# Kernel optimization log

Measured on AMD Instinct MI355X. Metric: run time of the kernel, lower is better.

Reference implementation:

```python
import jax, jax.numpy as jnp
import numpy as np

B, S, HID = 2, 2048, 1024
H, KVH, D = 16, 4, 64
N_REP = H // KVH
SCALE = D ** -0.5
CAP = 50.0


def rotate_half(x):
    x1, x2 = x[..., : D // 2], x[..., D // 2 :]
    return jnp.concatenate((-x2, x1), axis=-1)


def setup_inputs() -> dict:
    key = jax.random.key(0)
    ks = jax.random.split(key, 10)
    X = jax.random.normal(ks[0], (B, S, HID), dtype=jnp.float32)
    # RoPE tables: (B, S, D)
    inv_freq = 1.0 / (10000.0 ** (np.arange(0, D, 2, dtype=np.float32) / D))
    pos = np.arange(S, dtype=np.float32)
    freqs = np.outer(pos, inv_freq)  # (S, D/2)
    emb = np.concatenate([freqs, freqs], axis=-1)  # (S, D)
    cos = jnp.broadcast_to(jnp.asarray(np.cos(emb)), (B, S, D))
    sin = jnp.broadcast_to(jnp.asarray(np.sin(emb)), (B, S, D))
    # causal mask: 1 where key <= query
    mask = jnp.broadcast_to(jnp.tril(jnp.ones((S, S), dtype=jnp.int32)), (B, S, S))
    std = HID ** -0.5
    Wq = jax.random.normal(ks[1], (HID, HID), dtype=jnp.float32) * std
    bq = jnp.zeros((HID,), dtype=jnp.float32)
    Wk = jax.random.normal(ks[2], (KVH * D, HID), dtype=jnp.float32) * std
    bk = jnp.zeros((KVH * D,), dtype=jnp.float32)
    Wv = jax.random.normal(ks[3], (KVH * D, HID), dtype=jnp.float32) * std
    bv = jnp.zeros((KVH * D,), dtype=jnp.float32)
    Wo = jax.random.normal(ks[4], (HID, HID), dtype=jnp.float32) * std
    bo = jnp.zeros((HID,), dtype=jnp.float32)
    return {"X": X, "cos": cos, "sin": sin, "mask": mask,
            "Wq": Wq, "bq": bq, "Wk": Wk, "bk": bk,
            "Wv": Wv, "bv": bv, "Wo": Wo, "bo": bo}


def reference(X, cos, sin, mask, Wq, bq, Wk, bk, Wv, bv, Wo, bo):
    bsz, q_len, _ = X.shape
    q = (X @ Wq.T + bq).reshape(bsz, q_len, H, D).transpose(0, 2, 1, 3)    # (B,H,S,D)
    k = (X @ Wk.T + bk).reshape(bsz, q_len, KVH, D).transpose(0, 2, 1, 3)  # (B,KVH,S,D)
    v = (X @ Wv.T + bv).reshape(bsz, q_len, KVH, D).transpose(0, 2, 1, 3)
    c = cos[:, None, :, :]  # (B,1,S,D)
    s = sin[:, None, :, :]
    q = q * c + rotate_half(q) * s
    k = k * c + rotate_half(k) * s
    k = jnp.repeat(k, N_REP, axis=1)  # GQA expand -> (B,H,S,D)
    v = jnp.repeat(v, N_REP, axis=1)
    scores = jnp.einsum('bhqd,bhkd->bhqk', q, k) * SCALE
    scores = jnp.clip(scores, -CAP, CAP)  # attention cap
    scores = jnp.where(mask[:, None, :, :] == 0, -1e9, scores)
    attn = jax.nn.softmax(scores, axis=-1)  # dropout p=0 -> identity
    ctx = jnp.einsum('bhqk,bhkd->bhqd', attn, v)
    ctx = ctx.transpose(0, 2, 1, 3).reshape(bsz, q_len, H * D)
    out = ctx @ Wo.T + bo
    return (out, attn)
```

## Files before the change

kernel.cpp:

```cpp
#include <hip/hip_runtime.h>
#include <cstdint>
#include <cstddef>

#define S_LEN   2048
#define BATCH   2
#define HID_DIM 1024
#define NHEAD   16
#define NKV     4
#define DHEAD   64
#define SCALE_F 0.125f
#define L2E     1.44269504f
#define QSCALE  (SCALE_F * L2E)
#define CAPL2   (50.0f * L2E)

typedef unsigned short u16;
typedef __attribute__((ext_vector_type(8))) short  short8_t;
typedef __attribute__((ext_vector_type(4))) float  f32x4;
typedef __attribute__((ext_vector_type(4))) u16    u16x4;

static __device__ __forceinline__ u16 f2bf(float f) {
  uint32_t x = __builtin_bit_cast(uint32_t, f);
  x += 0x7fffu + ((x >> 16) & 1u);
  return (u16)(x >> 16);
}

static __device__ __forceinline__ void gload_lds16(const void* g, void* l) {
  __builtin_amdgcn_global_load_lds((const __attribute__((address_space(1))) void*)g,
                                   (__attribute__((address_space(3))) void*)l, 16, 0, 0);
}

static __device__ __forceinline__ float expclamp2(float x) {
  return __builtin_amdgcn_exp2f(__builtin_amdgcn_fmed3f(x, -CAPL2, CAPL2) - CAPL2);
}

__global__ void cast_all(const float* __restrict__ X,  u16* __restrict__ xb,
                         const float* __restrict__ Wq, u16* __restrict__ wqb,
                         const float* __restrict__ Wk, u16* __restrict__ wkb,
                         const float* __restrict__ Wv, u16* __restrict__ wvb,
                         const float* __restrict__ Wo, u16* __restrict__ wob) {
  const float* src; u16* dst; int n4;
  switch (blockIdx.y) {
    case 0:  src = X;  dst = xb;  n4 = (BATCH * S_LEN * HID_DIM) / 4; break;
    case 1:  src = Wq; dst = wqb; n4 = (HID_DIM * HID_DIM) / 4;       break;
    case 2:  src = Wk; dst = wkb; n4 = (NKV * DHEAD * HID_DIM) / 4;   break;
    case 3:  src = Wv; dst = wvb; n4 = (NKV * DHEAD * HID_DIM) / 4;   break;
    default: src = Wo; dst = wob; n4 = (HID_DIM * HID_DIM) / 4;       break;
  }
  for (int i = blockIdx.x * 256 + threadIdx.x; i < n4; i += gridDim.x * 256) {
    f32x4 v = ((const f32x4*)src)[i];
    u16x4 o;
    o[0] = f2bf(v[0]); o[1] = f2bf(v[1]); o[2] = f2bf(v[2]); o[3] = f2bf(v[3]);
    ((u16x4*)dst)[i] = o;
  }
}

__global__ __launch_bounds__(256) void gemm_qkv(const u16* __restrict__ Xb,
                                                const u16* __restrict__ Wqb,
                                                const u16* __restrict__ Wkb,
                                                const u16* __restrict__ Wvb,
                                                const float* __restrict__ bq,
                                                const float* __restrict__ bk,
                                                const float* __restrict__ bv,
                                                const float* __restrict__ cosb,
                                                const float* __restrict__ sinb,
                                                u16* __restrict__ qout,
                                                u16* __restrict__ kout,
                                                u16* __restrict__ vtout) {
  __shared__ u16 As[128 * 64];
  __shared__ u16 Bs[128 * 64];
  const int tid = threadIdx.x, lane = tid & 63, wid = tid >> 6;
  const int l15 = lane & 15, lg = lane >> 4;
  const int m0 = blockIdx.x * 128, n0 = blockIdx.y * 128;
  const int wm = wid & 1, wn = wid >> 1;
  const int K = HID_DIM;

  const u16* Wp; const float* biasp; int nl, mode;
  if (n0 < 1024)      { Wp = Wqb; biasp = bq; nl = n0;        mode = 0; }
  else if (n0 < 1280) { Wp = Wkb; biasp = bk; nl = n0 - 1024; mode = 1; }
  else                { Wp = Wvb; biasp = bv; nl = n0 - 1280; mode = 2; }

  f32x4 acc[4][4];
  #pragma unroll
  for (int a = 0; a < 4; ++a)
    #pragma unroll
    for (int b2 = 0; b2 < 4; ++b2) acc[a][b2] = (f32x4){0.f, 0.f, 0.f, 0.f};

  const int srow = (lane >> 3), sg = (lane & 7);

  for (int kk = 0; kk < K; kk += 64) {
    __syncthreads();
    #pragma unroll
    for (int i = 0; i < 4; ++i) {
      const int c = wid * 4 + i;
      const int r = c * 8 + srow;
      const int g = sg ^ (r & 7);
      gload_lds16(Xb + (size_t)(m0 + r) * K + kk + g * 8, As + c * 512);
      gload_lds16(Wp + (size_t)(nl + r) * K + kk + g * 8, Bs + c * 512);
    }
    __syncthreads();
    #pragma unroll
    for (int ks = 0; ks < 2; ++ks) {
      short8_t xa[4], wb[4];
      #pragma unroll
      for (int f = 0; f < 4; ++f) {
        const int rm = wm * 64 + f * 16 + l15;
        const int rn = wn * 64 + f * 16 + l15;
        xa[f] = *(const short8_t*)(As + rm * 64 + (((ks * 4 + lg) ^ (rm & 7)) * 8));
        wb[f] = *(const short8_t*)(Bs + rn * 64 + (((ks * 4 + lg) ^ (rn & 7)) * 8));
      }
      if (mode != 2) {
        #pragma unroll
        for (int fn = 0; fn < 4; ++fn)
          #pragma unroll
          for (int fm = 0; fm < 4; ++fm)
            acc[fn][fm] = __builtin_amdgcn_mfma_f32_16x16x32_bf16(wb[fn], xa[fm], acc[fn][fm], 0, 0, 0);
      } else {
        #pragma unroll
        for (int fn = 0; fn < 4; ++fn)
          #pragma unroll
          for (int fm = 0; fm < 4; ++fm)
            acc[fn][fm] = __builtin_amdgcn_mfma_f32_16x16x32_bf16(xa[fm], wb[fn], acc[fn][fm], 0, 0, 0);
      }
    }
  }

  const int m_base = m0 + wm * 64;
  const int nlb = nl + wn * 64;

  if (mode < 2) {
    const int Nout = (mode == 0) ? HID_DIM : (NKV * DHEAD);
    const float qs = (mode == 0) ? QSCALE : 1.0f;
    u16* outb = (mode == 0) ? qout : kout;
    #pragma unroll
    for (int fm = 0; fm < 4; ++fm) {
      const int row = m_base + fm * 16 + l15;
      #pragma unroll
      for (int fn = 0; fn < 2; ++fn) {
        const int dh = fn * 16 + lg * 4;
        const f32x4 c4 = *(const f32x4*)(cosb + (size_t)row * 64 + dh);
        const f32x4 s4 = *(const f32x4*)(sinb + (size_t)row * 64 + dh);
        f32x4 x1 = acc[fn][fm]     + *(const f32x4*)(biasp + nlb + fn * 16 + lg * 4);
        f32x4 x2 = acc[fn + 2][fm] + *(const f32x4*)(biasp + nlb + (fn + 2) * 16 + lg * 4);
        f32x4 o1 = (x1 * c4 - x2 * s4) * qs;
        f32x4 o2 = (x2 * c4 + x1 * s4) * qs;
        u16x4 u1, u2;
        #pragma unroll
        for (int i = 0; i < 4; ++i) { u1[i] = f2bf(o1[i]); u2[i] = f2bf(o2[i]); }
        *(u16x4*)(outb + (size_t)row * Nout + nlb + fn * 16 + lg * 4)       = u1;
        *(u16x4*)(outb + (size_t)row * Nout + nlb + (fn + 2) * 16 + lg * 4) = u2;
      }
    }
  } else {
    #pragma unroll
    for (int fn = 0; fn < 4; ++fn) {
      const int d = nlb + fn * 16 + l15;
      const float bvs = biasp[d];
      #pragma unroll
      for (int fm = 0; fm < 4; ++fm) {
        const int s0 = m_base + fm * 16 + lg * 4;
        const int b_ = s0 >> 11, s_ = s0 & (S_LEN - 1);
        u16x4 o;
        #pragma unroll
        for (int i = 0; i < 4; ++i) o[i] = f2bf(acc[fn][fm][i] + bvs);
        *(u16x4*)(vtout + (size_t)(b_ * 256 + d) * S_LEN + s_) = o;
      }
    }
  }
}

__global__ __launch_bounds__(256) void gemm_out(const u16* __restrict__ A,
                                                const u16* __restrict__ W,
                                                const float* __restrict__ bias,
                                                float* __restrict__ outp) {
  __shared__ u16 As[128 * 64];
  __shared__ u16 Bs[128 * 64];
  const int tid = threadIdx.x, lane = tid & 63, wid = tid >> 6;
  const int l15 = lane & 15, lg = lane >> 4;
  const int m0 = blockIdx.x * 128, n0 = blockIdx.y * 128;
  const int wm = wid & 1, wn = wid >> 1;
  const int K = HID_DIM, N = HID_DIM;

  f32x4 acc[4][4];
  #pragma unroll
  for (int a = 0; a < 4; ++a)
    #pragma unroll
    for (int b2 = 0; b2 < 4; ++b2) acc[a][b2] = (f32x4){0.f, 0.f, 0.f, 0.f};

  const int srow = (lane >> 3), sg = (lane & 7);

  for (int kk = 0; kk < K; kk += 64) {
    __syncthreads();
    #pragma unroll
    for (int i = 0; i < 4; ++i) {
      const int c = wid * 4 + i;
      const int r = c * 8 + srow;
      const int g = sg ^ (r & 7);
      gload_lds16(A + (size_t)(m0 + r) * K + kk + g * 8, As + c * 512);
      gload_lds16(W + (size_t)(n0 + r) * K + kk + g * 8, Bs + c * 512);
    }
    __syncthreads();
    #pragma unroll
    for (int ks = 0; ks < 2; ++ks) {
      short8_t xa[4], wb[4];
      #pragma unroll
      for (int f = 0; f < 4; ++f) {
        const int rm = wm * 64 + f * 16 + l15;
        const int rn = wn * 64 + f * 16 + l15;
        xa[f] = *(const short8_t*)(As + rm * 64 + (((ks * 4 + lg) ^ (rm & 7)) * 8));
        wb[f] = *(const short8_t*)(Bs + rn * 64 + (((ks * 4 + lg) ^ (rn & 7)) * 8));
      }
      #pragma unroll
      for (int fn = 0; fn < 4; ++fn)
        #pragma unroll
        for (int fm = 0; fm < 4; ++fm)
          acc[fn][fm] = __builtin_amdgcn_mfma_f32_16x16x32_bf16(wb[fn], xa[fm], acc[fn][fm], 0, 0, 0);
    }
  }

  const int m_base = m0 + wm * 64, n_base = n0 + wn * 64;
  #pragma unroll
  for (int fn = 0; fn < 4; ++fn) {
    const int col = n_base + fn * 16 + lg * 4;
    const f32x4 bvv = *(const f32x4*)(bias + col);
    #pragma unroll
    for (int fm = 0; fm < 4; ++fm) {
      const int row = m_base + fm * 16 + l15;
      *(f32x4*)(outp + (size_t)row * N + col) = acc[fn][fm] + bvv;
    }
  }
}

__global__ __launch_bounds__(256) void attn_fused(const u16* __restrict__ qb,
                                                  const u16* __restrict__ kb,
                                                  const u16* __restrict__ vtb,
                                                  float* __restrict__ attn,
                                                  u16* __restrict__ ctxb) {
  __shared__ u16 kS[2][64 * 64];
  __shared__ u16 vS[2][64 * 64];
  __shared__ u16 pS[4][16][72];

  const int tid = threadIdx.x, lane = tid & 63, wid = tid >> 6;
  const int l15 = lane & 15, lg = lane >> 4;
  const int bh = blockIdx.x, b = bh >> 4, h = bh & 15, kvh = h >> 2;
  const int qt = (int)(gridDim.y - 1 - blockIdx.y);
  const int q0 = qt * 64;
  const int NT = qt + 1;
  const int qw = q0 + wid * 16;
  const int qrow = qw + l15;

  const u16* qp = qb + (size_t)(b * S_LEN + qrow) * HID_DIM + h * DHEAD + lg * 8;
  const short8_t qf0 = *(const short8_t*)qp;
  const short8_t qf1 = *(const short8_t*)(qp + 32);

  const u16* kbase  = kb  + (size_t)(b * S_LEN) * (NKV * DHEAD) + kvh * DHEAD;
  const u16* vtbase = vtb + (size_t)(b * NKV + kvh) * DHEAD * S_LEN;

  const int sr8 = wid * 8 + (lane >> 3);
  const int sgr = lane & 7;

  auto stageK = [&](int bi, int kv0) {
    #pragma unroll
    for (int it = 0; it < 2; ++it) {
      const int r = it * 32 + sr8;
      const int g = sgr ^ (r & 7);
      gload_lds16(kbase + (size_t)(kv0 + r) * (NKV * DHEAD) + g * 8,
                  &kS[bi][(it * 32 + wid * 8) * 64]);
    }
  };
  auto stageV = [&](int bi, int kv0) {
    #pragma unroll
    for (int it = 0; it < 2; ++it) {
      const int r = it * 32 + sr8;
      const int g = sgr ^ (r & 7);
      gload_lds16(vtbase + (size_t)r * S_LEN + kv0 + g * 8,
                  &vS[bi][(it * 32 + wid * 8) * 64]);
    }
  };

  f32x4 lacc = (f32x4){0.f, 0.f, 0.f, 0.f};
  stageK(0, 0);
  for (int t = 0; t < NT; ++t) {
    const int kv0 = t * 64;
    if (t + 1 < NT) {
      stageK((t + 1) & 1, kv0 + 64);
      asm volatile("s_waitcnt vmcnt(2)" ::: "memory");
    } else {
      asm volatile("s_waitcnt vmcnt(0)" ::: "memory");
    }
    __builtin_amdgcn_s_barrier();
    const u16* ks = kS[t & 1];
    const bool maskc = (kv0 + 63 > qw);
    #pragma unroll
    for (int g16 = 0; g16 < 4; ++g16) {
      const int r = g16 * 16 + l15;
      short8_t ka0 = *(const short8_t*)(ks + r * 64 + ((lg ^ (r & 7)) * 8));
      short8_t ka1 = *(const short8_t*)(ks + r * 64 + (((4 + lg) ^ (r & 7)) * 8));
      f32x4 sacc = (f32x4){0.f, 0.f, 0.f, 0.f};
      sacc = __builtin_amdgcn_mfma_f32_16x16x32_bf16(ka0, qf0, sacc, 0, 0, 0);
      sacc = __builtin_amdgcn_mfma_f32_16x16x32_bf16(ka1, qf1, sacc, 0, 0, 0);
      #pragma unroll
      for (int i = 0; i < 4; ++i) {
        float e = expclamp2(sacc[i]);
        if (maskc) {
          const int kvi = kv0 + g16 * 16 + lg * 4 + i;
          e = (kvi <= qrow) ? e : 0.f;
        }
        lacc[i] += e;
      }
    }
    __builtin_amdgcn_s_barrier();
  }
  float lsum = (lacc[0] + lacc[1]) + (lacc[2] + lacc[3]);
  lsum += __shfl_xor(lsum, 16);
  lsum += __shfl_xor(lsum, 32);
  const float invl = 1.f / lsum;

  float* abase = attn + (size_t)bh * S_LEN * S_LEN;
  float* arow  = abase + (size_t)qrow * S_LEN;
  f32x4 ctx[4];
  #pragma unroll
  for (int dt = 0; dt < 4; ++dt) ctx[dt] = (f32x4){0.f, 0.f, 0.f, 0.f};

  stageK(0, 0);
  stageV(0, 0);
  for (int t = 0; t < NT; ++t) {
    const int kv0 = t * 64;
    if (t + 1 < NT) {
      stageK((t + 1) & 1, kv0 + 64);
      stageV((t + 1) & 1, kv0 + 64);
      asm volatile("s_waitcnt vmcnt(4)" ::: "memory");
    } else {
      asm volatile("s_waitcnt vmcnt(0)" ::: "memory");
    }
    __builtin_amdgcn_s_barrier();
    const u16* ks = kS[t & 1];
    const u16* vs = vS[t & 1];
    const bool maskc = (kv0 + 63 > qw);
    #pragma unroll
    for (int g16 = 0; g16 < 4; ++g16) {
      const int r = g16 * 16 + l15;
      short8_t ka0 = *(const short8_t*)(ks + r * 64 + ((lg ^ (r & 7)) * 8));
      short8_t ka1 = *(const short8_t*)(ks + r * 64 + (((4 + lg) ^ (r & 7)) * 8));
      f32x4 sacc = (f32x4){0.f, 0.f, 0.f, 0.f};
      sacc = __builtin_amdgcn_mfma_f32_16x16x32_bf16(ka0, qf0, sacc, 0, 0, 0);
      sacc = __builtin_amdgcn_mfma_f32_16x16x32_bf16(ka1, qf1, sacc, 0, 0, 0);
      f32x4 pv; u16x4 pb;
      #pragma unroll
      for (int i = 0; i < 4; ++i) {
        float e = expclamp2(sacc[i]);
        if (maskc) {
          const int kvi = kv0 + g16 * 16 + lg * 4 + i;
          e = (kvi <= qrow) ? e : 0.f;
        }
        float p = e * invl;
        pv[i] = p;
        pb[i] = f2bf(p);
      }
      *(f32x4*)(arow + kv0 + g16 * 16 + lg * 4) = pv;
      *(u16x4*)&pS[wid][l15][g16 * 16 + lg * 4] = pb;
    }
    short8_t pa0 = *(const short8_t*)&pS[wid][l15][lg * 8];
    short8_t pa1 = *(const short8_t*)&pS[wid][l15][32 + lg * 8];
    #pragma unroll
    for (int dt = 0; dt < 4; ++dt) {
      const int r = dt * 16 + l15;
      short8_t bv0 = *(const short8_t*)(vs + r * 64 + ((lg ^ (r & 7)) * 8));
      short8_t bv1 = *(const short8_t*)(vs + r * 64 + (((4 + lg) ^ (r & 7)) * 8));
      ctx[dt] = __builtin_amdgcn_mfma_f32_16x16x32_bf16(bv0, pa0, ctx[dt], 0, 0, 0);
      ctx[dt] = __builtin_amdgcn_mfma_f32_16x16x32_bf16(bv1, pa1, ctx[dt], 0, 0, 0);
    }
    __builtin_amdgcn_s_barrier();
  }

  #pragma unroll
  for (int dt = 0; dt < 4; ++dt) {
    u16x4 o;
    #pragma unroll
    for (int i = 0; i < 4; ++i) o[i] = f2bf(ctx[dt][i]);
    *(u16x4*)(ctxb + (size_t)(b * S_LEN + qrow) * HID_DIM + h * DHEAD + dt * 16 + lg * 4) = o;
  }

  const int zc0 = q0 + 64;
  if (zc0 < S_LEN) {
    const f32x4 z = (f32x4){0.f, 0.f, 0.f, 0.f};
    for (int r = wid; r < 64; r += 4) {
      float* rowp = abase + (size_t)(q0 + r) * S_LEN;
      for (int c = zc0 + lane * 4; c < S_LEN; c += 256)
        *(f32x4*)(rowp + c) = z;
    }
  }
}

extern "C" void kernel_launch(void* const* d_in, const int* in_sizes, int n_in,
                              void* d_out, int out_size, void* d_ws, size_t ws_size,
                              hipStream_t stream) {
  (void)in_sizes; (void)n_in; (void)out_size; (void)ws_size;
  const float* X    = (const float*)d_in[0];
  const float* cosb = (const float*)d_in[1];
  const float* sinb = (const float*)d_in[2];
  const float* Wq = (const float*)d_in[4];
  const float* bq = (const float*)d_in[5];
  const float* Wk = (const float*)d_in[6];
  const float* bk = (const float*)d_in[7];
  const float* Wv = (const float*)d_in[8];
  const float* bv = (const float*)d_in[9];
  const float* Wo = (const float*)d_in[10];
  const float* bo = (const float*)d_in[11];

  float* outp  = (float*)d_out;
  float* attnp = outp + (size_t)BATCH * S_LEN * HID_DIM;

  const int M = BATCH * S_LEN;
  u16* ws    = (u16*)d_ws;
  u16* Xb    = ws;
  u16* Wqb   = Xb  + (size_t)M * HID_DIM;
  u16* Wkb   = Wqb + (size_t)HID_DIM * HID_DIM;
  u16* Wvb   = Wkb + (size_t)NKV * DHEAD * HID_DIM;
  u16* Wob   = Wvb + (size_t)NKV * DHEAD * HID_DIM;
  u16* qbuf  = Wob + (size_t)HID_DIM * HID_DIM;
  u16* kbuf  = qbuf + (size_t)M * HID_DIM;
  u16* vtbuf = kbuf + (size_t)M * NKV * DHEAD;
  u16* ctxb  = vtbuf + (size_t)M * NKV * DHEAD;

  cast_all<<<dim3(1024, 5), 256, 0, stream>>>(X, Xb, Wq, Wqb, Wk, Wkb, Wv, Wvb, Wo, Wob);

  gemm_qkv<<<dim3(M / 128, 12), 256, 0, stream>>>(Xb, Wqb, Wkb, Wvb, bq, bk, bv,
                                                  cosb, sinb, qbuf, kbuf, vtbuf);

  attn_fused<<<dim3(BATCH * NHEAD, S_LEN / 64), 256, 0, stream>>>(qbuf, kbuf, vtbuf, attnp, ctxb);

  gemm_out<<<dim3(M / 128, HID_DIM / 128), 256, 0, stream>>>(ctxb, Wob, bo, outp);
}
```

Before: 235.9 us.

## Process two 64-row query sub-tiles per attention block to reuse K/V tiles

Each attention workgroup now handles 128 query rows, split into two 64-row sub-tiles A and B, so every staged K/V tile in shared memory feeds twice as many MFMAs. This halves the grid and the redundant global-to-LDS K/V traffic. Sub-tile A skips compute on fully masked KV tiles and writes zeros to the attention matrix there instead. The trade-offs are more registers per thread, fewer blocks (reduced occupancy and parallelism), and worse load balance across the causal triangle.

```diff
diff --git a/kernel.cpp b/kernel.cpp
--- a/kernel.cpp
+++ b/kernel.cpp
@@ -237,20 +237,23 @@
                                                   u16* __restrict__ ctxb) {
   __shared__ u16 kS[2][64 * 64];
   __shared__ u16 vS[2][64 * 64];
-  __shared__ u16 pS[4][16][72];
+  __shared__ u16 pS[4][2][16][72];
 
   const int tid = threadIdx.x, lane = tid & 63, wid = tid >> 6;
   const int l15 = lane & 15, lg = lane >> 4;
   const int bh = blockIdx.x, b = bh >> 4, h = bh & 15, kvh = h >> 2;
   const int qt = (int)(gridDim.y - 1 - blockIdx.y);
-  const int q0 = qt * 64;
-  const int NT = qt + 1;
-  const int qw = q0 + wid * 16;
-  const int qrow = qw + l15;
-
-  const u16* qp = qb + (size_t)(b * S_LEN + qrow) * HID_DIM + h * DHEAD + lg * 8;
-  const short8_t qf0 = *(const short8_t*)qp;
-  const short8_t qf1 = *(const short8_t*)(qp + 32);
+  const int q0 = qt * 128;
+  const int NT = 2 * qt + 2;
+  const int qwA = q0 + wid * 16;
+  const int qwB = qwA + 64;
+
+  const u16* qpA = qb + (size_t)(b * S_LEN + qwA + l15) * HID_DIM + h * DHEAD + lg * 8;
+  const u16* qpB = qb + (size_t)(b * S_LEN + qwB + l15) * HID_DIM + h * DHEAD + lg * 8;
+  const short8_t qfA0 = *(const short8_t*)qpA;
+  const short8_t qfA1 = *(const short8_t*)(qpA + 32);
+  const short8_t qfB0 = *(const short8_t*)qpB;
+  const short8_t qfB1 = *(const short8_t*)(qpB + 32);
 
   const u16* kbase  = kb  + (size_t)(b * S_LEN) * (NKV * DHEAD) + kvh * DHEAD;
   const u16* vtbase = vtb + (size_t)(b * NKV + kvh) * DHEAD * S_LEN;
@@ -277,7 +280,8 @@
     }
   };
 
-  f32x4 lacc = (f32x4){0.f, 0.f, 0.f, 0.f};
+  f32x4 laccA = (f32x4){0.f, 0.f, 0.f, 0.f};
+  f32x4 laccB = (f32x4){0.f, 0.f, 0.f, 0.f};
   stageK(0, 0);
   for (int t = 0; t < NT; ++t) {
     const int kv0 = t * 64;
@@ -289,37 +293,58 @@
     }
     __builtin_amdgcn_s_barrier();
     const u16* ks = kS[t & 1];
-    const bool maskc = (kv0 + 63 > qw);
+    const bool actA = (kv0 <= qwA + 15);
+    const bool mA = (kv0 + 63 > qwA), mB = (kv0 + 63 > qwB);
     #pragma unroll
     for (int g16 = 0; g16 < 4; ++g16) {
       const int r = g16 * 16 + l15;
       short8_t ka0 = *(const short8_t*)(ks + r * 64 + ((lg ^ (r & 7)) * 8));
       short8_t ka1 = *(const short8_t*)(ks + r * 64 + (((4 + lg) ^ (r & 7)) * 8));
-      f32x4 sacc = (f32x4){0.f, 0.f, 0.f, 0.f};
-      sacc = __builtin_amdgcn_mfma_f32_16x16x32_bf16(ka0, qf0, sacc, 0, 0, 0);
-      sacc = __builtin_amdgcn_mfma_f32_16x16x32_bf16(ka1, qf1, sacc, 0, 0, 0);
+      f32x4 sB = (f32x4){0.f, 0.f, 0.f, 0.f};
+      sB = __builtin_amdgcn_mfma_f32_16x16x32_bf16(ka0, qfB0, sB, 0, 0, 0);
+      sB = __builtin_amdgcn_mfma_f32_16x16x32_bf16(ka1, qfB1, sB, 0, 0, 0);
       #pragma unroll
       for (int i = 0; i < 4; ++i) {
-        float e = expclamp2(sacc[i]);
-        if (maskc) {
+        float e = expclamp2(sB[i]);
+        if (mB) {
           const int kvi = kv0 + g16 * 16 + lg * 4 + i;
-          e = (kvi <= qrow) ? e : 0.f;
+          e = (kvi <= qwB + l15) ? e : 0.f;
         }
-        lacc[i] += e;
+        laccB[i] += e;
+      }
+      if (actA) {
+        f32x4 sA = (f32x4){0.f, 0.f, 0.f, 0.f};
+        sA = __builtin_amdgcn_mfma_f32_16x16x32_bf16(ka0, qfA0, sA, 0, 0, 0);
+        sA = __builtin_amdgcn_mfma_f32_16x16x32_bf16(ka1, qfA1, sA, 0, 0, 0);
+        #pragma unroll
+        for (int i = 0; i < 4; ++i) {
+          float e = expclamp2(sA[i]);
+          if (mA) {
+            const int kvi = kv0 + g16 * 16 + lg * 4 + i;
+            e = (kvi <= qwA + l15) ? e : 0.f;
+          }
+          laccA[i] += e;
+        }
       }
     }
     __builtin_amdgcn_s_barrier();
   }
-  float lsum = (lacc[0] + lacc[1]) + (lacc[2] + lacc[3]);
-  lsum += __shfl_xor(lsum, 16);
-  lsum += __shfl_xor(lsum, 32);
-  const float invl = 1.f / lsum;
+  float lsA = (laccA[0] + laccA[1]) + (laccA[2] + laccA[3]);
+  float lsB = (laccB[0] + laccB[1]) + (laccB[2] + laccB[3]);
+  lsA += __shfl_xor(lsA, 16); lsA += __shfl_xor(lsA, 32);
+  lsB += __shfl_xor(lsB, 16); lsB += __shfl_xor(lsB, 32);
+  const float invlA = 1.f / lsA;
+  const float invlB = 1.f / lsB;
 
   float* abase = attn + (size_t)bh * S_LEN * S_LEN;
-  float* arow  = abase + (size_t)qrow * S_LEN;
-  f32x4 ctx[4];
+  float* arowA = abase + (size_t)(qwA + l15) * S_LEN;
+  float* arowB = abase + (size_t)(qwB + l15) * S_LEN;
+  f32x4 ctxA[4], ctxB[4];
   #pragma unroll
-  for (int dt = 0; dt < 4; ++dt) ctx[dt] = (f32x4){0.f, 0.f, 0.f, 0.f};
+  for (int dt = 0; dt < 4; ++dt) {
+    ctxA[dt] = (f32x4){0.f, 0.f, 0.f, 0.f};
+    ctxB[dt] = (f32x4){0.f, 0.f, 0.f, 0.f};
+  }
 
   stageK(0, 0);
   stageV(0, 0);
@@ -335,55 +360,88 @@
     __builtin_amdgcn_s_barrier();
     const u16* ks = kS[t & 1];
     const u16* vs = vS[t & 1];
-    const bool maskc = (kv0 + 63 > qw);
+    const bool actA = (kv0 <= qwA + 15);
+    const bool mA = (kv0 + 63 > qwA), mB = (kv0 + 63 > qwB);
+
     #pragma unroll
     for (int g16 = 0; g16 < 4; ++g16) {
       const int r = g16 * 16 + l15;
       short8_t ka0 = *(const short8_t*)(ks + r * 64 + ((lg ^ (r & 7)) * 8));
       short8_t ka1 = *(const short8_t*)(ks + r * 64 + (((4 + lg) ^ (r & 7)) * 8));
-      f32x4 sacc = (f32x4){0.f, 0.f, 0.f, 0.f};
-      sacc = __builtin_amdgcn_mfma_f32_16x16x32_bf16(ka0, qf0, sacc, 0, 0, 0);
-      sacc = __builtin_amdgcn_mfma_f32_16x16x32_bf16(ka1, qf1, sacc, 0, 0, 0);
+      f32x4 sB = (f32x4){0.f, 0.f, 0.f, 0.f};
+      sB = __builtin_amdgcn_mfma_f32_16x16x32_bf16(ka0, qfB0, sB, 0, 0, 0);
+      sB = __builtin_amdgcn_mfma_f32_16x16x32_bf16(ka1, qfB1, sB, 0, 0, 0);
       f32x4 pv; u16x4 pb;
       #pragma unroll
       for (int i = 0; i < 4; ++i) {
-        float e = expclamp2(sacc[i]);
-        if (maskc) {
+        float e = expclamp2(sB[i]);
+        if (mB) {
           const int kvi = kv0 + g16 * 16 + lg * 4 + i;
-          e = (kvi <= qrow) ? e : 0.f;
+          e = (kvi <= qwB + l15) ? e : 0.f;
         }
-        float p = e * invl;
-        pv[i] = p;
-        pb[i] = f2bf(p);
-      }
-      *(f32x4*)(arow + kv0 + g16 * 16 + lg * 4) = pv;
-      *(u16x4*)&pS[wid][l15][g16 * 16 + lg * 4] = pb;
-    }
-    short8_t pa0 = *(const short8_t*)&pS[wid][l15][lg * 8];
-    short8_t pa1 = *(const short8_t*)&pS[wid][l15][32 + lg * 8];
+        float p = e * invlB;
+        pv[i] = p; pb[i] = f2bf(p);
+      }
+      *(f32x4*)(arowB + kv0 + g16 * 16 + lg * 4) = pv;
+      *(u16x4*)&pS[wid][1][l15][g16 * 16 + lg * 4] = pb;
+
+      if (actA) {
+        f32x4 sA = (f32x4){0.f, 0.f, 0.f, 0.f};
+        sA = __builtin_amdgcn_mfma_f32_16x16x32_bf16(ka0, qfA0, sA, 0, 0, 0);
+        sA = __builtin_amdgcn_mfma_f32_16x16x32_bf16(ka1, qfA1, sA, 0, 0, 0);
+        #pragma unroll
+        for (int i = 0; i < 4; ++i) {
+          float e = expclamp2(sA[i]);
+          if (mA) {
+            const int kvi = kv0 + g16 * 16 + lg * 4 + i;
+            e = (kvi <= qwA + l15) ? e : 0.f;
+          }
+          float p = e * invlA;
+          pv[i] = p; pb[i] = f2bf(p);
+        }
+        *(f32x4*)(arowA + kv0 + g16 * 16 + lg * 4) = pv;
+        *(u16x4*)&pS[wid][0][l15][g16 * 16 + lg * 4] = pb;
+      } else {
+        const f32x4 z = (f32x4){0.f, 0.f, 0.f, 0.f};
+        *(f32x4*)(arowA + kv0 + g16 * 16 + lg * 4) = z;
+      }
+    }
+
+    short8_t paB0 = *(const short8_t*)&pS[wid][1][l15][lg * 8];
+    short8_t paB1 = *(const short8_t*)&pS[wid][1][l15][32 + lg * 8];
+    short8_t paA0, paA1;
+    if (actA) {
+      paA0 = *(const short8_t*)&pS[wid][0][l15][lg * 8];
+      paA1 = *(const short8_t*)&pS[wid][0][l15][32 + lg * 8];
+    }
     #pragma unroll
     for (int dt = 0; dt < 4; ++dt) {
       const int r = dt * 16 + l15;
       short8_t bv0 = *(const short8_t*)(vs + r * 64 + ((lg ^ (r & 7)) * 8));
       short8_t bv1 = *(const short8_t*)(vs + r * 64 + (((4 + lg) ^ (r & 7)) * 8));
-      ctx[dt] = __builtin_amdgcn_mfma_f32_16x16x32_bf16(bv0, pa0, ctx[dt], 0, 0, 0);
-      ctx[dt] = __builtin_amdgcn_mfma_f32_16x16x32_bf16(bv1, pa1, ctx[dt], 0, 0, 0);
+      ctxB[dt] = __builtin_amdgcn_mfma_f32_16x16x32_bf16(bv0, paB0, ctxB[dt], 0, 0, 0);
+      ctxB[dt] = __builtin_amdgcn_mfma_f32_16x16x32_bf16(bv1, paB1, ctxB[dt], 0, 0, 0);
+      if (actA) {
+        ctxA[dt] = __builtin_amdgcn_mfma_f32_16x16x32_bf16(bv0, paA0, ctxA[dt], 0, 0, 0);
+        ctxA[dt] = __builtin_amdgcn_mfma_f32_16x16x32_bf16(bv1, paA1, ctxA[dt], 0, 0, 0);
+      }
     }
     __builtin_amdgcn_s_barrier();
   }
 
   #pragma unroll
   for (int dt = 0; dt < 4; ++dt) {
-    u16x4 o;
-    #pragma unroll
-    for (int i = 0; i < 4; ++i) o[i] = f2bf(ctx[dt][i]);
-    *(u16x4*)(ctxb + (size_t)(b * S_LEN + qrow) * HID_DIM + h * DHEAD + dt * 16 + lg * 4) = o;
-  }
-
-  const int zc0 = q0 + 64;
+    u16x4 oA, oB;
+    #pragma unroll
+    for (int i = 0; i < 4; ++i) { oA[i] = f2bf(ctxA[dt][i]); oB[i] = f2bf(ctxB[dt][i]); }
+    *(u16x4*)(ctxb + (size_t)(b * S_LEN + qwA + l15) * HID_DIM + h * DHEAD + dt * 16 + lg * 4) = oA;
+    *(u16x4*)(ctxb + (size_t)(b * S_LEN + qwB + l15) * HID_DIM + h * DHEAD + dt * 16 + lg * 4) = oB;
+  }
+
+  const int zc0 = q0 + 128;
   if (zc0 < S_LEN) {
     const f32x4 z = (f32x4){0.f, 0.f, 0.f, 0.f};
-    for (int r = wid; r < 64; r += 4) {
+    for (int r = wid; r < 128; r += 4) {
       float* rowp = abase + (size_t)(q0 + r) * S_LEN;
       for (int c = zc0 + lane * 4; c < S_LEN; c += 256)
         *(f32x4*)(rowp + c) = z;
@@ -427,7 +485,7 @@
   gemm_qkv<<<dim3(M / 128, 12), 256, 0, stream>>>(Xb, Wqb, Wkb, Wvb, bq, bk, bv,
                                                   cosb, sinb, qbuf, kbuf, vtbuf);
 
-  attn_fused<<<dim3(BATCH * NHEAD, S_LEN / 64), 256, 0, stream>>>(qbuf, kbuf, vtbuf, attnp, ctxb);
+  attn_fused<<<dim3(BATCH * NHEAD, S_LEN / 128), 256, 0, stream>>>(qbuf, kbuf, vtbuf, attnp, ctxb);
 
   gemm_out<<<dim3(M / 128, HID_DIM / 128), 256, 0, stream>>>(ctxb, Wob, bo, outp);
 }
```

After: 239.3 us. Within noise of the previous version (+1.5%).

## Split attention row-sum pass into separate kernel with wider K tiles

Applied to the files above, without the earlier changes.

Moves the first pass of the two-pass softmax, which computes per-row exp sums, out of the fused attention kernel into its own kernel. That kernel uses 128-row K tiles and writes reciprocal row sums to workspace, and the attention kernel reads them back. The goal is to make the write-heavy probability/PV kernel lighter and let the sum pass run with less staging overhead. It also drops the constant subtraction inside the clamped exp2 and folds the normalisation multiply before masking. The cost is an extra launch, a second read of Q and K, and a small workspace buffer.

```diff
diff --git a/kernel.cpp b/kernel.cpp
--- a/kernel.cpp
+++ b/kernel.cpp
@@ -29,8 +29,8 @@
                                    (__attribute__((address_space(3))) void*)l, 16, 0, 0);
 }
 
-static __device__ __forceinline__ float expclamp2(float x) {
-  return __builtin_amdgcn_exp2f(__builtin_amdgcn_fmed3f(x, -CAPL2, CAPL2) - CAPL2);
+static __device__ __forceinline__ float exp2med3(float x) {
+  return __builtin_amdgcn_exp2f(__builtin_amdgcn_fmed3f(x, -CAPL2, CAPL2));
 }
 
 __global__ void cast_all(const float* __restrict__ X,  u16* __restrict__ xb,
@@ -230,9 +230,82 @@
   }
 }
 
+__global__ __launch_bounds__(256) void lsum_kernel(const u16* __restrict__ qb,
+                                                   const u16* __restrict__ kb,
+                                                   float* __restrict__ invlp) {
+  __shared__ u16 kS[2][128 * 64];
+
+  const int tid = threadIdx.x, lane = tid & 63, wid = tid >> 6;
+  const int l15 = lane & 15, lg = lane >> 4;
+  const int bh = blockIdx.x, b = bh >> 4, h = bh & 15, kvh = h >> 2;
+  const int qt = (int)(gridDim.y - 1 - blockIdx.y);
+  const int qw = qt * 64 + wid * 16;
+  const int qrow = qw + l15;
+  const int NT = (qt + 2) >> 1;
+
+  const u16* qp = qb + (size_t)(b * S_LEN + qrow) * HID_DIM + h * DHEAD + lg * 8;
+  const short8_t qf0 = *(const short8_t*)qp;
+  const short8_t qf1 = *(const short8_t*)(qp + 32);
+
+  const u16* kbase = kb + (size_t)(b * S_LEN) * (NKV * DHEAD) + kvh * DHEAD;
+
+  const int sr8 = wid * 8 + (lane >> 3);
+  const int sgr = lane & 7;
+
+  auto stageK = [&](int bi, int kv0) {
+    #pragma unroll
+    for (int it = 0; it < 4; ++it) {
+      const int r = it * 32 + sr8;
+      const int g = sgr ^ (r & 7);
+      gload_lds16(kbase + (size_t)(kv0 + r) * (NKV * DHEAD) + g * 8,
+                  &kS[bi][(it * 32 + wid * 8) * 64]);
+    }
+  };
+
+  f32x4 lacc = (f32x4){0.f, 0.f, 0.f, 0.f};
+  stageK(0, 0);
+  for (int t = 0; t < NT; ++t) {
+    const int kv0 = t * 128;
+    if (t + 1 < NT) {
+      stageK((t + 1) & 1, kv0 + 128);
+      asm volatile("s_waitcnt vmcnt(4)" ::: "memory");
+    } else {
+      asm volatile("s_waitcnt vmcnt(0)" ::: "memory");
+    }
+    __builtin_amdgcn_s_barrier();
+    const u16* ks = kS[t & 1];
+    const bool maskc = (kv0 + 127 > qw);
+    #pragma unroll
+    for (int g16 = 0; g16 < 8; ++g16) {
+      const int r = g16 * 16 + l15;
+      short8_t ka0 = *(const short8_t*)(ks + r * 64 + ((lg ^ (r & 7)) * 8));
+      short8_t ka1 = *(const short8_t*)(ks + r * 64 + (((4 + lg) ^ (r & 7)) * 8));
+      f32x4 sacc = (f32x4){0.f, 0.f, 0.f, 0.f};
+      sacc = __builtin_amdgcn_mfma_f32_16x16x32_bf16(ka0, qf0, sacc, 0, 0, 0);
+      sacc = __builtin_amdgcn_mfma_f32_16x16x32_bf16(ka1, qf1, sacc, 0, 0, 0);
+      #pragma unroll
+      for (int i = 0; i < 4; ++i) {
+        float e = exp2med3(sacc[i]);
+        if (maskc) {
+          const int kvi = kv0 + g16 * 16 + lg * 4 + i;
+          e = (kvi <= qrow) ? e : 0.f;
+        }
+        lacc[i] += e;
+      }
+    }
+    __builtin_amdgcn_s_barrier();
+  }
+  float ls = (lacc[0] + lacc[1]) + (lacc[2] + lacc[3]);
+  ls += __shfl_xor(ls, 16);
+  ls += __shfl_xor(ls, 32);
+  if (lg == 0)
+    invlp[(size_t)bh * S_LEN + qrow] = 1.f / ls;
+}
+
 __global__ __launch_bounds__(256) void attn_fused(const u16* __restrict__ qb,
                                                   const u16* __restrict__ kb,
                                                   const u16* __restrict__ vtb,
+                                                  const float* __restrict__ invlp,
                                                   float* __restrict__ attn,
                                                   u16* __restrict__ ctxb) {
   __shared__ u16 kS[2][64 * 64];
@@ -251,6 +324,7 @@
   const u16* qp = qb + (size_t)(b * S_LEN + qrow) * HID_DIM + h * DHEAD + lg * 8;
   const short8_t qf0 = *(const short8_t*)qp;
   const short8_t qf1 = *(const short8_t*)(qp + 32);
+  const float invl = invlp[(size_t)bh * S_LEN + qrow];
 
   const u16* kbase  = kb  + (size_t)(b * S_LEN) * (NKV * DHEAD) + kvh * DHEAD;
   const u16* vtbase = vtb + (size_t)(b * NKV + kvh) * DHEAD * S_LEN;
@@ -276,44 +350,6 @@
                   &vS[bi][(it * 32 + wid * 8) * 64]);
     }
   };
-
-  f32x4 lacc = (f32x4){0.f, 0.f, 0.f, 0.f};
-  stageK(0, 0);
-  for (int t = 0; t < NT; ++t) {
-    const int kv0 = t * 64;
-    if (t + 1 < NT) {
-      stageK((t + 1) & 1, kv0 + 64);
-      asm volatile("s_waitcnt vmcnt(2)" ::: "memory");
-    } else {
-      asm volatile("s_waitcnt vmcnt(0)" ::: "memory");
-    }
-    __builtin_amdgcn_s_barrier();
-    const u16* ks = kS[t & 1];
-    const bool maskc = (kv0 + 63 > qw);
-    #pragma unroll
-    for (int g16 = 0; g16 < 4; ++g16) {
-      const int r = g16 * 16 + l15;
-      short8_t ka0 = *(const short8_t*)(ks + r * 64 + ((lg ^ (r & 7)) * 8));
-      short8_t ka1 = *(const short8_t*)(ks + r * 64 + (((4 + lg) ^ (r & 7)) * 8));
-      f32x4 sacc = (f32x4){0.f, 0.f, 0.f, 0.f};
-      sacc = __builtin_amdgcn_mfma_f32_16x16x32_bf16(ka0, qf0, sacc, 0, 0, 0);
-      sacc = __builtin_amdgcn_mfma_f32_16x16x32_bf16(ka1, qf1, sacc, 0, 0, 0);
-      #pragma unroll
-      for (int i = 0; i < 4; ++i) {
-        float e = expclamp2(sacc[i]);
-        if (maskc) {
-          const int kvi = kv0 + g16 * 16 + lg * 4 + i;
-          e = (kvi <= qrow) ? e : 0.f;
-        }
-        lacc[i] += e;
-      }
-    }
-    __builtin_amdgcn_s_barrier();
-  }
-  float lsum = (lacc[0] + lacc[1]) + (lacc[2] + lacc[3]);
-  lsum += __shfl_xor(lsum, 16);
-  lsum += __shfl_xor(lsum, 32);
-  const float invl = 1.f / lsum;
 
   float* abase = attn + (size_t)bh * S_LEN * S_LEN;
   float* arow  = abase + (size_t)qrow * S_LEN;
@@ -347,12 +383,11 @@
       f32x4 pv; u16x4 pb;
       #pragma unroll
       for (int i = 0; i < 4; ++i) {
-        float e = expclamp2(sacc[i]);
+        float p = exp2med3(sacc[i]) * invl;
         if (maskc) {
           const int kvi = kv0 + g16 * 16 + lg * 4 + i;
-          e = (kvi <= qrow) ? e : 0.f;
+          p = (kvi <= qrow) ? p : 0.f;
         }
-        float p = e * invl;
         pv[i] = p;
         pb[i] = f2bf(p);
       }
@@ -421,13 +456,17 @@
   u16* kbuf  = qbuf + (size_t)M * HID_DIM;
   u16* vtbuf = kbuf + (size_t)M * NKV * DHEAD;
   u16* ctxb  = vtbuf + (size_t)M * NKV * DHEAD;
+  float* invlp = (float*)(ctxb + (size_t)M * HID_DIM);
 
   cast_all<<<dim3(1024, 5), 256, 0, stream>>>(X, Xb, Wq, Wqb, Wk, Wkb, Wv, Wvb, Wo, Wob);
 
   gemm_qkv<<<dim3(M / 128, 12), 256, 0, stream>>>(Xb, Wqb, Wkb, Wvb, bq, bk, bv,
                                                   cosb, sinb, qbuf, kbuf, vtbuf);
 
-  attn_fused<<<dim3(BATCH * NHEAD, S_LEN / 64), 256, 0, stream>>>(qbuf, kbuf, vtbuf, attnp, ctxb);
+  lsum_kernel<<<dim3(BATCH * NHEAD, S_LEN / 64), 256, 0, stream>>>(qbuf, kbuf, invlp);
+
+  attn_fused<<<dim3(BATCH * NHEAD, S_LEN / 64), 256, 0, stream>>>(qbuf, kbuf, vtbuf,
+                                                                  invlp, attnp, ctxb);
 
   gemm_out<<<dim3(M / 128, HID_DIM / 128), 256, 0, stream>>>(ctxb, Wob, bo, outp);
 }
```

Result: slower. 244.0 us (+3.5%).

## Single-buffer V tile, overlap V load with score pass, raise occupancy hint

Applied to the files above, without the earlier changes.

In the second attention pass the V tile drops its double buffer. It is now loaded at the start of each iteration, so the load overlaps the score, exp and probability-store work, with a wait and barrier placed just before the PV MFMAs. The kernel gets a launch_bounds occupancy hint of 4 blocks, and the exp helper drops the constant offset subtraction. The normalisation multiply is also moved ahead of the mask select. The intent is to cut LDS usage and hide V load latency. In exchange, the new vmcnt waits also cover the outstanding attention stores, which may serialise memory traffic, and an extra full wait per iteration reduces how much the K prefetch can overlap.

```diff
diff --git a/kernel.cpp b/kernel.cpp
--- a/kernel.cpp
+++ b/kernel.cpp
@@ -29,8 +29,8 @@
                                    (__attribute__((address_space(3))) void*)l, 16, 0, 0);
 }
 
-static __device__ __forceinline__ float expclamp2(float x) {
-  return __builtin_amdgcn_exp2f(__builtin_amdgcn_fmed3f(x, -CAPL2, CAPL2) - CAPL2);
+static __device__ __forceinline__ float exp2med3(float x) {
+  return __builtin_amdgcn_exp2f(__builtin_amdgcn_fmed3f(x, -CAPL2, CAPL2));
 }
 
 __global__ void cast_all(const float* __restrict__ X,  u16* __restrict__ xb,
@@ -230,13 +230,13 @@
   }
 }
 
-__global__ __launch_bounds__(256) void attn_fused(const u16* __restrict__ qb,
-                                                  const u16* __restrict__ kb,
-                                                  const u16* __restrict__ vtb,
-                                                  float* __restrict__ attn,
-                                                  u16* __restrict__ ctxb) {
+__global__ __launch_bounds__(256, 4) void attn_fused(const u16* __restrict__ qb,
+                                                     const u16* __restrict__ kb,
+                                                     const u16* __restrict__ vtb,
+                                                     float* __restrict__ attn,
+                                                     u16* __restrict__ ctxb) {
   __shared__ u16 kS[2][64 * 64];
-  __shared__ u16 vS[2][64 * 64];
+  __shared__ u16 vS[64 * 64];
   __shared__ u16 pS[4][16][72];
 
   const int tid = threadIdx.x, lane = tid & 63, wid = tid >> 6;
@@ -267,13 +267,13 @@
                   &kS[bi][(it * 32 + wid * 8) * 64]);
     }
   };
-  auto stageV = [&](int bi, int kv0) {
+  auto stageV = [&](int kv0) {
     #pragma unroll
     for (int it = 0; it < 2; ++it) {
       const int r = it * 32 + sr8;
       const int g = sgr ^ (r & 7);
       gload_lds16(vtbase + (size_t)r * S_LEN + kv0 + g * 8,
-                  &vS[bi][(it * 32 + wid * 8) * 64]);
+                  &vS[(it * 32 + wid * 8) * 64]);
     }
   };
 
@@ -300,7 +300,7 @@
       sacc = __builtin_amdgcn_mfma_f32_16x16x32_bf16(ka1, qf1, sacc, 0, 0, 0);
       #pragma unroll
       for (int i = 0; i < 4; ++i) {
-        float e = expclamp2(sacc[i]);
+        float e = exp2med3(sacc[i]);
         if (maskc) {
           const int kvi = kv0 + g16 * 16 + lg * 4 + i;
           e = (kvi <= qrow) ? e : 0.f;
@@ -322,19 +322,16 @@
   for (int dt = 0; dt < 4; ++dt) ctx[dt] = (f32x4){0.f, 0.f, 0.f, 0.f};
 
   stageK(0, 0);
-  stageV(0, 0);
+  asm volatile("s_waitcnt vmcnt(0)" ::: "memory");
+  __builtin_amdgcn_s_barrier();
+
   for (int t = 0; t < NT; ++t) {
     const int kv0 = t * 64;
-    if (t + 1 < NT) {
-      stageK((t + 1) & 1, kv0 + 64);
-      stageV((t + 1) & 1, kv0 + 64);
-      asm volatile("s_waitcnt vmcnt(4)" ::: "memory");
-    } else {
-      asm volatile("s_waitcnt vmcnt(0)" ::: "memory");
-    }
-    __builtin_amdgcn_s_barrier();
+    stageV(kv0);
+    const bool pre = (t + 1 < NT);
+    if (pre) stageK((t + 1) & 1, kv0 + 64);
+
     const u16* ks = kS[t & 1];
-    const u16* vs = vS[t & 1];
     const bool maskc = (kv0 + 63 > qw);
     #pragma unroll
     for (int g16 = 0; g16 < 4; ++g16) {
@@ -347,28 +344,34 @@
       f32x4 pv; u16x4 pb;
       #pragma unroll
       for (int i = 0; i < 4; ++i) {
-        float e = expclamp2(sacc[i]);
+        float p = exp2med3(sacc[i]) * invl;
         if (maskc) {
           const int kvi = kv0 + g16 * 16 + lg * 4 + i;
-          e = (kvi <= qrow) ? e : 0.f;
+          p = (kvi <= qrow) ? p : 0.f;
         }
-        float p = e * invl;
         pv[i] = p;
         pb[i] = f2bf(p);
       }
       *(f32x4*)(arow + kv0 + g16 * 16 + lg * 4) = pv;
       *(u16x4*)&pS[wid][l15][g16 * 16 + lg * 4] = pb;
     }
+
+    if (pre) asm volatile("s_waitcnt vmcnt(2)" ::: "memory");
+    else     asm volatile("s_waitcnt vmcnt(0)" ::: "memory");
+    __builtin_amdgcn_s_barrier();
+
     short8_t pa0 = *(const short8_t*)&pS[wid][l15][lg * 8];
     short8_t pa1 = *(const short8_t*)&pS[wid][l15][32 + lg * 8];
     #pragma unroll
     for (int dt = 0; dt < 4; ++dt) {
       const int r = dt * 16 + l15;
-      short8_t bv0 = *(const short8_t*)(vs + r * 64 + ((lg ^ (r & 7)) * 8));
-      short8_t bv1 = *(const short8_t*)(vs + r * 64 + (((4 + lg) ^ (r & 7)) * 8));
+      short8_t bv0 = *(const short8_t*)(vS + r * 64 + ((lg ^ (r & 7)) * 8));
+      short8_t bv1 = *(const short8_t*)(vS + r * 64 + (((4 + lg) ^ (r & 7)) * 8));
       ctx[dt] = __builtin_amdgcn_mfma_f32_16x16x32_bf16(bv0, pa0, ctx[dt], 0, 0, 0);
       ctx[dt] = __builtin_amdgcn_mfma_f32_16x16x32_bf16(bv1, pa1, ctx[dt], 0, 0, 0);
     }
+
+    asm volatile("s_waitcnt vmcnt(0)" ::: "memory");
     __builtin_amdgcn_s_barrier();
   }
 
```

Result: faster. 231.2 us (-2.0%).
